# Performance work log

Hardware: AMD Instinct MI355X
Metric: run time of the kernel (lower is better)

The kernel has to match this reference:

```python
import jax, jax.numpy as jnp
import numpy as np

EPS = 1e-6
ROPE_THETA = 1000000.0

def _rmsnorm(x, scale):
    var = jnp.mean(jnp.square(x), axis=-1, keepdims=True)
    return x * jax.lax.rsqrt(var + EPS) * scale

def _rope(x, positions):
    # x: [B, h, T, H]; GPT-NeoX style rotate-half
    H = x.shape[-1]
    half = H // 2
    inv_freq = 1.0 / (ROPE_THETA ** (jnp.arange(half, dtype=jnp.float32) * 2.0 / H))
    ang = positions.astype(jnp.float32)[:, None] * inv_freq[None, :]  # [T, half]
    cos, sin = jnp.cos(ang), jnp.sin(ang)
    x1, x2 = x[..., :half], x[..., half:]
    return jnp.concatenate([x1 * cos - x2 * sin, x2 * cos + x1 * sin], axis=-1)

def setup_inputs() -> dict:
    key = jax.random.key(0)
    ks = jax.random.split(key, 16)
    B, T, D = 2, 2048, 2048
    N, K, H = 16, 2, 128
    I = 5504
    s = 0.02
    return {
        "x": jax.random.normal(ks[0], (B, T, D), jnp.float32),
        "positions": jnp.arange(T, dtype=jnp.int32),
        "ln1_scale": jnp.ones((D,), jnp.float32),
        "q_w": jax.random.normal(ks[1], (N, D, H), jnp.float32) * s,
        "q_b": jax.random.normal(ks[2], (N, H), jnp.float32) * s,
        "k_w": jax.random.normal(ks[3], (K, D, H), jnp.float32) * s,
        "k_b": jax.random.normal(ks[4], (K, H), jnp.float32) * s,
        "v_w": jax.random.normal(ks[5], (K, D, H), jnp.float32) * s,
        "v_b": jax.random.normal(ks[6], (K, H), jnp.float32) * s,
        "o_w": jax.random.normal(ks[7], (N, H, D), jnp.float32) * s,
        "ln2_scale": jnp.ones((D,), jnp.float32),
        "gate_w": jax.random.normal(ks[8], (D, I), jnp.float32) * s,
        "up_w": jax.random.normal(ks[9], (D, I), jnp.float32) * s,
        "down_w": jax.random.normal(ks[10], (I, D), jnp.float32) * s,
    }

def reference(x, positions, ln1_scale, q_w, q_b, k_w, k_b, v_w, v_b, o_w,
              ln2_scale, gate_w, up_w, down_w):
    B, T, D = x.shape
    N, _, H = q_w.shape
    K = k_w.shape[0]
    group = N // K

    h = _rmsnorm(x, ln1_scale)

    # Projections (per source einsums) + bias
    q = jnp.einsum('btd,ndh->bnth', h, q_w) + q_b[None, :, None, :]
    k = jnp.einsum('btd,kdh->bkth', h, k_w) + k_b[None, :, None, :]
    v = jnp.einsum('btd,kdh->bkth', h, v_w) + v_b[None, :, None, :]

    q = _rope(q, positions) * (H ** -0.5)
    k = _rope(k, positions)

    # GQA: expand kv heads to query heads
    k = jnp.repeat(k, group, axis=1)  # [B,N,T,H]
    v = jnp.repeat(v, group, axis=1)

    # Causal self-attention (prefill path: kv cache filled from k, v)
    scores = jnp.einsum('bnth,bnsh->bnts', q, k)
    causal = positions[:, None] >= positions[None, :]  # [T, T]
    scores = jnp.where(causal[None, None, :, :], scores, -jnp.inf)
    probs = jax.nn.softmax(scores, axis=-1)
    attn = jnp.einsum('bnts,bnsh->bnth', probs, v)

    o = jnp.einsum('bnth,nhd->btd', attn, o_w)

    # Residual + post-attn norm + SwiGLU MLP + residual
    res = o + x
    h2 = _rmsnorm(res, ln2_scale)
    fuse = jax.nn.silu(h2 @ gate_w) * (h2 @ up_w)
    return res + fuse @ down_w
```

## Files before the change

### kernel.cpp

```cpp
#include <hip/hip_runtime.h>
#include <cstdint>
#include <cstddef>

typedef unsigned short u16;
typedef __attribute__((ext_vector_type(8))) short short8;
typedef __attribute__((ext_vector_type(4))) float f32x4;

#define DEV __device__ __forceinline__

DEV float bf2f(u16 v) { union { unsigned u; float f; } x; x.u = ((unsigned)v) << 16; return x.f; }
DEV u16 f2bf(float f) {
  union { float f; unsigned u; } x; x.f = f;
  unsigned r = x.u + 0x7fffu + ((x.u >> 16) & 1u);
  return (u16)(r >> 16);
}

DEV void gload_lds16(const void* g, void* l) {
  __builtin_amdgcn_global_load_lds((const __attribute__((address_space(1))) void*)g,
                                   (__attribute__((address_space(3))) void*)l, 16, 0, 0);
}

#define BARRIER __builtin_amdgcn_s_barrier()
#define VM0 asm volatile("s_waitcnt vmcnt(0)" ::: "memory")
#define VM4 asm volatile("s_waitcnt vmcnt(4)" ::: "memory")

__global__ __launch_bounds__(256) void transpose_w_kernel(
    const float* __restrict__ in, u16* __restrict__ out, int R, int C, int mode)
{
  __shared__ float tile[64][65];
  const int tx = threadIdx.x, ty = threadIdx.y;
  const int c0 = blockIdx.x * 64, r0 = blockIdx.y * 64;
  const float* inb = in + (size_t)blockIdx.z * R * C;
  u16* outb = out + (size_t)blockIdx.z * R * C;
#pragma unroll
  for (int i = 0; i < 8; ++i) {
    const int r = ty + i * 8;
    const float2 v = *(const float2*)&inb[(size_t)(r0 + r) * C + c0 + tx * 2];
    tile[r][tx * 2] = v.x;
    tile[r][tx * 2 + 1] = v.y;
  }
  __syncthreads();
#pragma unroll
  for (int i = 0; i < 8; ++i) {
    const int jj = ty + i * 8;
    const int j = c0 + jj;
    const int prow = mode ? ((j >> 7) * 256 + (((j >> 5) & 3) << 6) + ((mode == 2) << 5) + (j & 31))
                          : j;
    const unsigned a = f2bf(tile[tx * 2][jj]);
    const unsigned b = f2bf(tile[tx * 2 + 1][jj]);
    *(unsigned*)&outb[(size_t)prow * R + r0 + tx * 2] = a | (b << 16);
  }
}

__global__ __launch_bounds__(256) void concat_bias_kernel(
    const float* __restrict__ qb, const float* __restrict__ kb,
    const float* __restrict__ vb, float* __restrict__ bias)
{
  const int i = blockIdx.x * 256 + threadIdx.x;
  if (i < 2048) bias[i] = qb[i];
  else if (i < 2304) bias[i] = kb[i - 2048];
  else if (i < 2560) bias[i] = vb[i - 2304];
}

__global__ __launch_bounds__(256) void rmsnorm_kernel(
    const float* __restrict__ x, const float* __restrict__ scale, u16* __restrict__ out)
{
  const int row = blockIdx.x, tid = threadIdx.x;
  const float* xr = x + (size_t)row * 2048;
  const float4 v0 = *(const float4*)&xr[tid * 8];
  const float4 v1 = *(const float4*)&xr[tid * 8 + 4];
  float ss = v0.x * v0.x + v0.y * v0.y + v0.z * v0.z + v0.w * v0.w +
             v1.x * v1.x + v1.y * v1.y + v1.z * v1.z + v1.w * v1.w;
#pragma unroll
  for (int d = 32; d > 0; d >>= 1) ss += __shfl_down(ss, d);
  __shared__ float red[4];
  if ((tid & 63) == 0) red[tid >> 6] = ss;
  __syncthreads();
  const float tot = red[0] + red[1] + red[2] + red[3];
  const float inv = rsqrtf(tot * (1.f / 2048.f) + 1e-6f);
  const float* sc = scale + tid * 8;
  short8 ov;
  ov[0] = (short)f2bf(v0.x * inv * sc[0]); ov[1] = (short)f2bf(v0.y * inv * sc[1]);
  ov[2] = (short)f2bf(v0.z * inv * sc[2]); ov[3] = (short)f2bf(v0.w * inv * sc[3]);
  ov[4] = (short)f2bf(v1.x * inv * sc[4]); ov[5] = (short)f2bf(v1.y * inv * sc[5]);
  ov[6] = (short)f2bf(v1.z * inv * sc[6]); ov[7] = (short)f2bf(v1.w * inv * sc[7]);
  *(short8*)&out[(size_t)row * 2048 + tid * 8] = ov;
}

template <int BM, int BN, int TB, int MODE, int GR>
__global__ __launch_bounds__(TB, 512 / TB) void gemm_conv_kernel(
    const u16* __restrict__ A, const u16* __restrict__ Bt,
    void* C, const float* __restrict__ aux, int N, int K, int lda, int ldb)
{
  constexpr int MFRAG = BM / 32;
  constexpr int AISS = BM * 8 / TB;
  constexpr int BISS = BN * 8 / TB;
  constexpr int WN = BN / 64;
  __shared__ __align__(16) u16 As[2][BM * 64];
  __shared__ __align__(16) u16 Bs[3][BN * 64];

  const int tid = threadIdx.x;
  const int wv = tid >> 6, lane = tid & 63, lo = lane & 15, hi = lane >> 4;
  const int wm = wv / WN, wn = wv % WN;

  const int nwg = (int)gridDim.x;
  const int id0 = (int)blockIdx.x;
  const int id = (id0 & 7) * (nwg >> 3) + (id0 >> 3);
  const int ncol = N / BN;
  const int rg = id % GR, cc = (id / GR) % ncol, gg = id / (GR * ncol);
  const int by = gg * GR + rg, bx = cc;
  const int row0 = by * BM, col0 = bx * BN;

  const f32x4 fz = {0.f, 0.f, 0.f, 0.f};
  f32x4 acc[MFRAG][4];
#pragma unroll
  for (int m = 0; m < MFRAG; ++m)
#pragma unroll
    for (int n = 0; n < 4; ++n) acc[m][n] = fz;

  const int nt = K >> 6;

  auto STAGE_A = [&](int kt, int ab) {
#pragma unroll
    for (int i = 0; i < AISS; ++i) {
      const int f = i * TB + tid;
      const int rp = f >> 3, sp = tid & 7;
      gload_lds16(A + (size_t)(row0 + rp) * lda + kt * 64 + ((sp ^ (rp & 7)) * 8),
                  (char*)&As[ab][0] + (i * TB + wv * 64) * 16);
    }
  };
  auto STAGE_B = [&](int kt, int bb) {
#pragma unroll
    for (int i = 0; i < BISS; ++i) {
      const int f = i * TB + tid;
      const int rp = f >> 3, sp = tid & 7;
      gload_lds16(Bt + (size_t)(col0 + rp) * ldb + kt * 64 + ((sp ^ (rp & 7)) * 8),
                  (char*)&Bs[bb][0] + (i * TB + wv * 64) * 16);
    }
  };

#define LDA8M(ARR, BUF, S, G)                                                    \
  _Pragma("unroll")                                                              \
  for (int mt = 0; mt < 4; ++mt) {                                               \
    const int r = wm * (BM / 2) + ((G) * 4 + mt) * 16 + lo;                      \
    ARR[mt] = *(const short8*)&As[BUF][r * 64 + (((S) * 4 + hi) ^ (r & 7)) * 8]; \
  }
#define LDB8M(ARR, BUF, S)                                                       \
  _Pragma("unroll")                                                              \
  for (int nn = 0; nn < 4; ++nn) {                                               \
    const int r = wn * 64 + nn * 16 + lo;                                        \
    ARR[nn] = *(const short8*)&Bs[BUF][r * 64 + (((S) * 4 + hi) ^ (r & 7)) * 8]; \
  }
#define MFMA16M(AR, BR, G)                                                       \
  __builtin_amdgcn_s_setprio(1);                                                 \
  _Pragma("unroll")                                                              \
  for (int mt = 0; mt < 4; ++mt)                                                 \
    _Pragma("unroll")                                                            \
    for (int nn = 0; nn < 4; ++nn)                                               \
      acc[(G) * 4 + mt][nn] = __builtin_amdgcn_mfma_f32_16x16x32_bf16(           \
          AR[mt], BR[nn], acc[(G) * 4 + mt][nn], 0, 0, 0);                       \
  __builtin_amdgcn_s_setprio(0);

  STAGE_A(0, 0); STAGE_B(0, 0); STAGE_B(1, 1);
  VM4; BARRIER;

  int ab = 0, bcur = 0;
  for (int t = 0; t < nt; ++t) {
    const bool preA = (t + 1 < nt);
    const bool preB = (t + 2 < nt);
    const int bs2 = (bcur >= 1) ? bcur - 1 : 2;
    if constexpr (BM == 256) {
      short8 a0[4], a1[4], b0[4], a2[4], a3[4], b1[4];
      LDA8M(a0, ab, 0, 0); LDA8M(a1, ab, 0, 1); LDB8M(b0, bcur, 0);
      LDA8M(a2, ab, 1, 0); LDA8M(a3, ab, 1, 1); LDB8M(b1, bcur, 1);
      if (preA) STAGE_A(t + 1, ab ^ 1);
      if (preB) STAGE_B(t + 2, bs2);
      MFMA16M(a0, b0, 0); MFMA16M(a1, b0, 1);
      MFMA16M(a2, b1, 0); MFMA16M(a3, b1, 1);
      if (preA) { if (preB) VM4; else VM0; }
      BARRIER;
    } else {
      short8 a0[4], b0[4], a1[4], b1[4];
      LDA8M(a0, ab, 0, 0); LDB8M(b0, bcur, 0);
      LDA8M(a1, ab, 1, 0); LDB8M(b1, bcur, 1);
      if (preA) STAGE_A(t + 1, ab ^ 1);
      if (preB) STAGE_B(t + 2, bs2);
      MFMA16M(a0, b0, 0);
      MFMA16M(a1, b1, 0);
      if (preA) { if (preB) VM4; else VM0; }
      BARRIER;
    }
    ab ^= 1;
    bcur = (bcur == 2) ? 0 : bcur + 1;
  }
#undef LDA8M
#undef LDB8M
#undef MFMA16M

  float* Cf = (float*)C;
  u16* Ch = (u16*)C;
  if constexpr (MODE == 4) {
    const int ldo = N >> 1;
#pragma unroll
    for (int fm = 0; fm < MFRAG; ++fm) {
#pragma unroll
      for (int nn = 0; nn < 2; ++nn) {
        const int fcol = (col0 >> 1) + wn * 32 + nn * 16 + lo;
#pragma unroll
        for (int j = 0; j < 4; ++j) {
          const int row = row0 + wm * (BM / 2) + fm * 16 + hi * 4 + j;
          const float g = acc[fm][nn][j];
          const float u = acc[fm][nn + 2][j];
          const float sg = g / (1.f + __builtin_amdgcn_exp2f(-1.4426950408889634f * g));
          Ch[(size_t)row * ldo + fcol] = f2bf(sg * u);
        }
      }
    }
  } else {
#pragma unroll
    for (int fm = 0; fm < MFRAG; ++fm) {
#pragma unroll
      for (int nn = 0; nn < 4; ++nn) {
        const int col = col0 + wn * 64 + nn * 16 + lo;
#pragma unroll
        for (int j = 0; j < 4; ++j) {
          const int row = row0 + wm * (BM / 2) + fm * 16 + hi * 4 + j;
          const size_t idx = (size_t)row * N + col;
          const float v = acc[fm][nn][j];
          if (MODE == 0) Cf[idx] = v + aux[col];
          else if (MODE == 1) Cf[idx] = v + aux[idx];
          else if (MODE == 2) Ch[idx] = f2bf(v);
          else Ch[idx] = f2bf(v + aux[col]);
        }
      }
    }
  }
}

__global__ __launch_bounds__(256) void rope_qkv_kernel(
    const u16* __restrict__ qkv, const int* __restrict__ pos,
    u16* __restrict__ Qb, u16* __restrict__ Kb, u16* __restrict__ Vt)
{
  const int idx = blockIdx.x * 256 + threadIdx.x;
  const int bt = idx / 1408;
  const int r = idx - bt * 1408;
  const int t = bt & 2047, b = bt >> 11;
  if (r < 1152) {
    const bool isq = r < 1024;
    const int rr = isq ? r : r - 1024;
    const int n = rr >> 6, hp = rr & 63;
    const u16* q = qkv + (size_t)bt * 2560 + (isq ? 0 : 2048) + n * 128 + hp;
    const float x1 = bf2f(q[0]);
    const float x2 = bf2f(q[64]);
    const float inv = exp2f((float)hp * (-19.931568569324174f / 64.f));
    const float ang = (float)pos[t] * inv;
    float s, c;
    sincosf(ang, &s, &c);
    const float sc = isq ? 0.08838834764831845f * 1.4426950408889634f : 1.f;
    const size_t base = isq ? (((size_t)(b * 16 + n) * 2048 + t) * 128 + hp)
                            : (((size_t)(b * 2 + n) * 2048 + t) * 128 + hp);
    u16* outp = isq ? Qb : Kb;
    outp[base] = f2bf((x1 * c - x2 * s) * sc);
    outp[base + 64] = f2bf((x2 * c + x1 * s) * sc);
  } else {
    const int rr = r - 1152;
    const int kh = rr >> 7, hh = rr & 127;
    Vt[((size_t)((b * 2 + kh) * 128 + hh)) * 2048 + t] =
        qkv[(size_t)bt * 2560 + 2304 + kh * 128 + hh];
  }
}

__global__ __launch_bounds__(512) void attn_kernel(
    const u16* __restrict__ Qb, const u16* __restrict__ Kb,
    const u16* __restrict__ Vt, u16* __restrict__ Out)
{
  __shared__ u16 Ks[2][128 * 128];
  __shared__ u16 Vs[2][128 * 128];
  __shared__ u16 Ps[8][16 * 128];
  const int tid = threadIdx.x;
  const int wave = tid >> 6, lane = tid & 63, lo = lane & 15, hi = lane >> 4;
  const int bn = blockIdx.x;
  const int b = bn >> 4, n = bn & 15, kh = n >> 3;

  const f32x4 fz = {0.f, 0.f, 0.f, 0.f};
  const u16* kg = Kb + (size_t)(b * 2 + kh) * 2048 * 128;
  const u16* vg = Vt + (size_t)(b * 2 + kh) * 128 * 2048;

  auto STAGE = [&](int buf, int s0) {
#pragma unroll
    for (int i = 0; i < 4; ++i) {
      const int gk = i * 512 + tid;
      const int rk = gk >> 4, gck = gk & 15;
      gload_lds16(kg + (size_t)(s0 + rk) * 128 + ((gck ^ (rk & 7)) * 8),
                  (char*)&Ks[buf][0] + (i * 512 + wave * 64) * 16);
      gload_lds16(vg + (size_t)rk * 2048 + s0 + ((gck ^ (rk & 7)) * 8),
                  (char*)&Vs[buf][0] + (i * 512 + wave * 64) * 16);
    }
  };

  auto processTile = [&](int q0) {
    const int nblk = q0 / 128 + 1;
    const u16* qptr = Qb + ((size_t)((b * 16 + n) * 2048) + q0 + wave * 16 + lo) * 128;
    short8 qf[4];
#pragma unroll
    for (int kc = 0; kc < 4; ++kc) qf[kc] = *(const short8*)&qptr[kc * 32 + hi * 8];

    float m_r[4], l_r[4];
    f32x4 oacc[8];
#pragma unroll
    for (int j = 0; j < 4; ++j) { m_r[j] = -1e30f; l_r[j] = 0.f; }
#pragma unroll
    for (int ht = 0; ht < 8; ++ht) oacc[ht] = fz;

    __syncthreads();
    STAGE(0, 0);
    __syncthreads();

    int cur = 0;
    for (int sb = 0; sb < nblk; ++sb) {
      const int s0 = sb * 128;
      if (sb + 1 < nblk) STAGE(cur ^ 1, s0 + 128);

      float sall[8][4];
      __builtin_amdgcn_s_setprio(1);
#pragma unroll
      for (int st = 0; st < 8; ++st) {
        f32x4 s = fz;
#pragma unroll
        for (int kc = 0; kc < 4; ++kc) {
          const int row = st * 16 + lo;
          const int cb = (kc * 64 + hi * 16) ^ ((lo & 7) << 4);
          short8 kf = *(const short8*)&Ks[cur][row * 128 + (cb >> 1)];
          s = __builtin_amdgcn_mfma_f32_16x16x32_bf16(qf[kc], kf, s, 0, 0, 0);
        }
#pragma unroll
        for (int j = 0; j < 4; ++j) sall[st][j] = s[j];
      }
      __builtin_amdgcn_s_setprio(0);

      if (s0 + 128 > q0) {
#pragma unroll
        for (int st = 0; st < 8; ++st) {
          const int sg = s0 + st * 16 + lo;
#pragma unroll
          for (int j = 0; j < 4; ++j) {
            const int qg = q0 + wave * 16 + hi * 4 + j;
            if (sg > qg) sall[st][j] = -1e30f;
          }
        }
      }

      float tmax[4];
#pragma unroll
      for (int j = 0; j < 4; ++j) {
        float t = fmaxf(fmaxf(fmaxf(sall[0][j], sall[1][j]), fmaxf(sall[2][j], sall[3][j])),
                        fmaxf(fmaxf(sall[4][j], sall[5][j]), fmaxf(sall[6][j], sall[7][j])));
        t = fmaxf(t, __shfl_xor(t, 1));
        t = fmaxf(t, __shfl_xor(t, 2));
        t = fmaxf(t, __shfl_xor(t, 4));
        t = fmaxf(t, __shfl_xor(t, 8));
        tmax[j] = t;
      }
      const bool defer = __all((tmax[0] - m_r[0] <= 8.f) & (tmax[1] - m_r[1] <= 8.f) &
                               (tmax[2] - m_r[2] <= 8.f) & (tmax[3] - m_r[3] <= 8.f));
      if (!defer) {
        float alpha[4];
#pragma unroll
        for (int j = 0; j < 4; ++j) {
          const float mnew = fmaxf(m_r[j], tmax[j]);
          alpha[j] = __builtin_amdgcn_exp2f(m_r[j] - mnew);
          m_r[j] = mnew;
          l_r[j] *= alpha[j];
        }
#pragma unroll
        for (int ht = 0; ht < 8; ++ht) {
#pragma unroll
          for (int j = 0; j < 4; ++j) oacc[ht][j] *= alpha[j];
        }
      }

      float rsum[4] = {0.f, 0.f, 0.f, 0.f};
#pragma unroll
      for (int st = 0; st < 8; ++st) {
#pragma unroll
        for (int j = 0; j < 4; ++j) {
          const float p = __builtin_amdgcn_exp2f(sall[st][j] - m_r[j]);
          rsum[j] += p;
          const int row = hi * 4 + j;
          const int cbp = (st * 32 + lo * 2) ^ ((row & 7) << 4);
          Ps[wave][row * 128 + (cbp >> 1)] = f2bf(p);
        }
      }
#pragma unroll
      for (int j = 0; j < 4; ++j) {
        float rs = rsum[j];
        rs += __shfl_xor(rs, 1);
        rs += __shfl_xor(rs, 2);
        rs += __shfl_xor(rs, 4);
        rs += __shfl_xor(rs, 8);
        l_r[j] += rs;
      }

      asm volatile("s_waitcnt lgkmcnt(0)" ::: "memory");
      __builtin_amdgcn_sched_barrier(0);

      short8 pf[4];
#pragma unroll
      for (int s = 0; s < 4; ++s) {
        const int pcb = (s * 64 + hi * 16) ^ ((lo & 7) << 4);
        pf[s] = *(const short8*)&Ps[wave][lo * 128 + (pcb >> 1)];
      }
      __builtin_amdgcn_s_setprio(1);
#pragma unroll
      for (int ht = 0; ht < 8; ++ht) {
        const int row = ht * 16 + lo;
#pragma unroll
        for (int s = 0; s < 4; ++s) {
          const int cb = (s * 64 + hi * 16) ^ ((row & 7) << 4);
          const short8 vf = *(const short8*)&Vs[cur][row * 128 + (cb >> 1)];
          oacc[ht] = __builtin_amdgcn_mfma_f32_16x16x32_bf16(pf[s], vf, oacc[ht], 0, 0, 0);
        }
      }
      __builtin_amdgcn_s_setprio(0);

      if (sb + 1 < nblk) __syncthreads();
      cur ^= 1;
    }

#pragma unroll
    for (int j = 0; j < 4; ++j) {
      const float inv = 1.0f / l_r[j];
      const int trow = q0 + wave * 16 + hi * 4 + j;
      const size_t base = ((size_t)(b * 2048 + trow)) * 2048 + n * 128;
#pragma unroll
      for (int ht = 0; ht < 8; ++ht)
        Out[base + ht * 16 + lo] = f2bf(oacc[ht][j] * inv);
    }
  };

  processTile((int)(15 - blockIdx.y) * 128);
  processTile((int)blockIdx.y * 128);
}

extern "C" void kernel_launch(void* const* d_in, const int* in_sizes, int n_in,
                              void* d_out, int out_size, void* d_ws, size_t ws_size,
                              hipStream_t stream)
{
  const float* x      = (const float*)d_in[0];
  const int*   pos    = (const int*)d_in[1];
  const float* ln1    = (const float*)d_in[2];
  const float* q_w    = (const float*)d_in[3];
  const float* q_b    = (const float*)d_in[4];
  const float* k_w    = (const float*)d_in[5];
  const float* k_b    = (const float*)d_in[6];
  const float* v_w    = (const float*)d_in[7];
  const float* v_b    = (const float*)d_in[8];
  const float* o_w    = (const float*)d_in[9];
  const float* ln2    = (const float*)d_in[10];
  const float* gate_w = (const float*)d_in[11];
  const float* up_w   = (const float*)d_in[12];
  const float* down_w = (const float*)d_in[13];
  float* out = (float*)d_out;

  char* w = (char*)d_ws;
  u16* wqkv_t = (u16*)w;       w += 2560LL * 2048 * 2;
  u16* o_wt   = (u16*)w;       w += 2048LL * 2048 * 2;
  u16* gu_t   = (u16*)w;       w += 11008LL * 2048 * 2;
  u16* d_t    = (u16*)w;       w += 2048LL * 5504 * 2;
  u16* hbuf   = (u16*)w;       w += 4096LL * 2048 * 2;
  float* bias_qkv = (float*)w; w += 2560 * 4;
  char* un = w;
  u16*  qkv   = (u16*)un;
  u16*  Qb    = (u16*)(un + 41943040LL);
  u16*  Kb    = (u16*)(un + 41943040LL + 16777216LL);
  u16*  Vt    = (u16*)(un + 41943040LL + 16777216LL + 2097152LL);
  u16*  attnb = (u16*)(un + 41943040LL + 16777216LL + 2097152LL + 2097152LL);
  u16*  fusebuf = (u16*)un;

  const dim3 tb(32, 8);
  transpose_w_kernel<<<dim3(2, 32, 16), tb, 0, stream>>>(q_w, wqkv_t, 2048, 128, 0);
  transpose_w_kernel<<<dim3(2, 32, 2),  tb, 0, stream>>>(k_w, wqkv_t + 2048LL * 2048, 2048, 128, 0);
  transpose_w_kernel<<<dim3(2, 32, 2),  tb, 0, stream>>>(v_w, wqkv_t + 2304LL * 2048, 2048, 128, 0);
  transpose_w_kernel<<<dim3(32, 32, 1), tb, 0, stream>>>(o_w, o_wt, 2048, 2048, 0);
  transpose_w_kernel<<<dim3(86, 32, 1), tb, 0, stream>>>(gate_w, gu_t, 2048, 5504, 1);
  transpose_w_kernel<<<dim3(86, 32, 1), tb, 0, stream>>>(up_w, gu_t, 2048, 5504, 2);
  transpose_w_kernel<<<dim3(32, 86, 1), tb, 0, stream>>>(down_w, d_t, 5504, 2048, 0);
  concat_bias_kernel<<<10, 256, 0, stream>>>(q_b, k_b, v_b, bias_qkv);

  rmsnorm_kernel<<<4096, 256, 0, stream>>>(x, ln1, hbuf);
  gemm_conv_kernel<128, 128, 256, 3, 8><<<640, 256, 0, stream>>>(hbuf, wqkv_t, qkv, bias_qkv, 2560, 2048, 2048, 2048);
  rope_qkv_kernel<<<22528, 256, 0, stream>>>(qkv, pos, Qb, Kb, Vt);
  attn_kernel<<<dim3(32, 8), 512, 0, stream>>>(Qb, Kb, Vt, attnb);
  gemm_conv_kernel<128, 128, 256, 1, 8><<<512, 256, 0, stream>>>(attnb, o_wt, out, x, 2048, 2048, 2048, 2048);
  rmsnorm_kernel<<<4096, 256, 0, stream>>>(out, ln2, hbuf);
  gemm_conv_kernel<256, 256, 512, 4, 4><<<688, 512, 0, stream>>>(hbuf, gu_t, fusebuf, nullptr, 11008, 2048, 2048, 2048);
  gemm_conv_kernel<128, 128, 256, 1, 2><<<512, 256, 0, stream>>>(fusebuf, d_t, out, out, 2048, 5504, 5504, 5504);
}
```

Measured before the change: 532.5 us.

## Switch GEMM inner loop to 32x32x16 bf16 MFMA with per-k-step fragment loads

Replaces the 16x16x32 MFMA tiling in the shared GEMM kernel with 32x32x16 MFMAs on 16-float accumulators, loading A/B fragments per k-substep of 16. The larger MFMA shape reuses each fragment load across more output elements, cutting LDS reads per flop. The epilogues are remapped to the 32x32 output layout. The down-projection launch also changes its row-group swizzle from 2 to 8, which alters L2 reuse.

```diff
diff --git a/kernel.cpp b/kernel.cpp
--- a/kernel.cpp
+++ b/kernel.cpp
@@ -5,6 +5,7 @@
 typedef unsigned short u16;
 typedef __attribute__((ext_vector_type(8))) short short8;
 typedef __attribute__((ext_vector_type(4))) float f32x4;
+typedef __attribute__((ext_vector_type(16))) float f32x16;
 
 #define DEV __device__ __forceinline__
 
@@ -92,15 +93,18 @@
     const u16* __restrict__ A, const u16* __restrict__ Bt,
     void* C, const float* __restrict__ aux, int N, int K, int lda, int ldb)
 {
-  constexpr int MFRAG = BM / 32;
+  constexpr int WN = BN / 64;
+  constexpr int NWM = (TB / 64) / WN;
+  constexpr int PWM = BM / NWM;
+  constexpr int AF = PWM / 32;
   constexpr int AISS = BM * 8 / TB;
   constexpr int BISS = BN * 8 / TB;
-  constexpr int WN = BN / 64;
   __shared__ __align__(16) u16 As[2][BM * 64];
   __shared__ __align__(16) u16 Bs[3][BN * 64];
 
   const int tid = threadIdx.x;
-  const int wv = tid >> 6, lane = tid & 63, lo = lane & 15, hi = lane >> 4;
+  const int wv = tid >> 6, lane = tid & 63;
+  const int l31 = lane & 31, l5 = lane >> 5;
   const int wm = wv / WN, wn = wv % WN;
 
   const int nwg = (int)gridDim.x;
@@ -111,12 +115,13 @@
   const int by = gg * GR + rg, bx = cc;
   const int row0 = by * BM, col0 = bx * BN;
 
-  const f32x4 fz = {0.f, 0.f, 0.f, 0.f};
-  f32x4 acc[MFRAG][4];
-#pragma unroll
-  for (int m = 0; m < MFRAG; ++m)
-#pragma unroll
-    for (int n = 0; n < 4; ++n) acc[m][n] = fz;
+  f32x16 acc[AF][2];
+#pragma unroll
+  for (int m = 0; m < AF; ++m)
+#pragma unroll
+    for (int n = 0; n < 2; ++n)
+#pragma unroll
+      for (int e = 0; e < 16; ++e) acc[m][n][e] = 0.f;
 
   const int nt = K >> 6;
 
@@ -139,28 +144,6 @@
     }
   };
 
-#define LDA8M(ARR, BUF, S, G)                                                    \
-  _Pragma("unroll")                                                              \
-  for (int mt = 0; mt < 4; ++mt) {                                               \
-    const int r = wm * (BM / 2) + ((G) * 4 + mt) * 16 + lo;                      \
-    ARR[mt] = *(const short8*)&As[BUF][r * 64 + (((S) * 4 + hi) ^ (r & 7)) * 8]; \
-  }
-#define LDB8M(ARR, BUF, S)                                                       \
-  _Pragma("unroll")                                                              \
-  for (int nn = 0; nn < 4; ++nn) {                                               \
-    const int r = wn * 64 + nn * 16 + lo;                                        \
-    ARR[nn] = *(const short8*)&Bs[BUF][r * 64 + (((S) * 4 + hi) ^ (r & 7)) * 8]; \
-  }
-#define MFMA16M(AR, BR, G)                                                       \
-  __builtin_amdgcn_s_setprio(1);                                                 \
-  _Pragma("unroll")                                                              \
-  for (int mt = 0; mt < 4; ++mt)                                                 \
-    _Pragma("unroll")                                                            \
-    for (int nn = 0; nn < 4; ++nn)                                               \
-      acc[(G) * 4 + mt][nn] = __builtin_amdgcn_mfma_f32_16x16x32_bf16(           \
-          AR[mt], BR[nn], acc[(G) * 4 + mt][nn], 0, 0, 0);                       \
-  __builtin_amdgcn_s_setprio(0);
-
   STAGE_A(0, 0); STAGE_B(0, 0); STAGE_B(1, 1);
   VM4; BARRIER;
 
@@ -169,64 +152,66 @@
     const bool preA = (t + 1 < nt);
     const bool preB = (t + 2 < nt);
     const int bs2 = (bcur >= 1) ? bcur - 1 : 2;
-    if constexpr (BM == 256) {
-      short8 a0[4], a1[4], b0[4], a2[4], a3[4], b1[4];
-      LDA8M(a0, ab, 0, 0); LDA8M(a1, ab, 0, 1); LDB8M(b0, bcur, 0);
-      LDA8M(a2, ab, 1, 0); LDA8M(a3, ab, 1, 1); LDB8M(b1, bcur, 1);
-      if (preA) STAGE_A(t + 1, ab ^ 1);
-      if (preB) STAGE_B(t + 2, bs2);
-      MFMA16M(a0, b0, 0); MFMA16M(a1, b0, 1);
-      MFMA16M(a2, b1, 0); MFMA16M(a3, b1, 1);
-      if (preA) { if (preB) VM4; else VM0; }
-      BARRIER;
-    } else {
-      short8 a0[4], b0[4], a1[4], b1[4];
-      LDA8M(a0, ab, 0, 0); LDB8M(b0, bcur, 0);
-      LDA8M(a1, ab, 1, 0); LDB8M(b1, bcur, 1);
-      if (preA) STAGE_A(t + 1, ab ^ 1);
-      if (preB) STAGE_B(t + 2, bs2);
-      MFMA16M(a0, b0, 0);
-      MFMA16M(a1, b1, 0);
-      if (preA) { if (preB) VM4; else VM0; }
-      BARRIER;
-    }
+#pragma unroll
+    for (int ks = 0; ks < 4; ++ks) {
+      short8 a[AF], b[2];
+#pragma unroll
+      for (int af = 0; af < AF; ++af) {
+        const int r = wm * PWM + af * 32 + l31;
+        a[af] = *(const short8*)&As[ab][r * 64 + (((ks * 2 + l5)) ^ (r & 7)) * 8];
+      }
+#pragma unroll
+      for (int bf = 0; bf < 2; ++bf) {
+        const int r = wn * 64 + bf * 32 + l31;
+        b[bf] = *(const short8*)&Bs[bcur][r * 64 + (((ks * 2 + l5)) ^ (r & 7)) * 8];
+      }
+      if (ks == 0) {
+        if (preA) STAGE_A(t + 1, ab ^ 1);
+        if (preB) STAGE_B(t + 2, bs2);
+      }
+      __builtin_amdgcn_s_setprio(1);
+#pragma unroll
+      for (int af = 0; af < AF; ++af) {
+#pragma unroll
+        for (int bf = 0; bf < 2; ++bf)
+          acc[af][bf] = __builtin_amdgcn_mfma_f32_32x32x16_bf16(
+              a[af], b[bf], acc[af][bf], 0, 0, 0);
+      }
+      __builtin_amdgcn_s_setprio(0);
+    }
+    if (preA) { if (preB) VM4; else VM0; }
+    BARRIER;
     ab ^= 1;
     bcur = (bcur == 2) ? 0 : bcur + 1;
   }
-#undef LDA8M
-#undef LDB8M
-#undef MFMA16M
 
   float* Cf = (float*)C;
   u16* Ch = (u16*)C;
   if constexpr (MODE == 4) {
     const int ldo = N >> 1;
-#pragma unroll
-    for (int fm = 0; fm < MFRAG; ++fm) {
-#pragma unroll
-      for (int nn = 0; nn < 2; ++nn) {
-        const int fcol = (col0 >> 1) + wn * 32 + nn * 16 + lo;
-#pragma unroll
-        for (int j = 0; j < 4; ++j) {
-          const int row = row0 + wm * (BM / 2) + fm * 16 + hi * 4 + j;
-          const float g = acc[fm][nn][j];
-          const float u = acc[fm][nn + 2][j];
-          const float sg = g / (1.f + __builtin_amdgcn_exp2f(-1.4426950408889634f * g));
-          Ch[(size_t)row * ldo + fcol] = f2bf(sg * u);
-        }
+    const int fcol = (col0 >> 1) + wn * 32 + l31;
+#pragma unroll
+    for (int af = 0; af < AF; ++af) {
+#pragma unroll
+      for (int reg = 0; reg < 16; ++reg) {
+        const int row = row0 + wm * PWM + af * 32 + (reg & 3) + 8 * (reg >> 2) + 4 * l5;
+        const float g = acc[af][0][reg];
+        const float u = acc[af][1][reg];
+        const float sg = g / (1.f + __builtin_amdgcn_exp2f(-1.4426950408889634f * g));
+        Ch[(size_t)row * ldo + fcol] = f2bf(sg * u);
       }
     }
   } else {
 #pragma unroll
-    for (int fm = 0; fm < MFRAG; ++fm) {
-#pragma unroll
-      for (int nn = 0; nn < 4; ++nn) {
-        const int col = col0 + wn * 64 + nn * 16 + lo;
-#pragma unroll
-        for (int j = 0; j < 4; ++j) {
-          const int row = row0 + wm * (BM / 2) + fm * 16 + hi * 4 + j;
+    for (int af = 0; af < AF; ++af) {
+#pragma unroll
+      for (int bf = 0; bf < 2; ++bf) {
+        const int col = col0 + wn * 64 + bf * 32 + l31;
+#pragma unroll
+        for (int reg = 0; reg < 16; ++reg) {
+          const int row = row0 + wm * PWM + af * 32 + (reg & 3) + 8 * (reg >> 2) + 4 * l5;
           const size_t idx = (size_t)row * N + col;
-          const float v = acc[fm][nn][j];
+          const float v = acc[af][bf][reg];
           if (MODE == 0) Cf[idx] = v + aux[col];
           else if (MODE == 1) Cf[idx] = v + aux[idx];
           else if (MODE == 2) Ch[idx] = f2bf(v);
@@ -494,5 +479,5 @@
   gemm_conv_kernel<128, 128, 256, 1, 8><<<512, 256, 0, stream>>>(attnb, o_wt, out, x, 2048, 2048, 2048, 2048);
   rmsnorm_kernel<<<4096, 256, 0, stream>>>(out, ln2, hbuf);
   gemm_conv_kernel<256, 256, 512, 4, 4><<<688, 512, 0, stream>>>(hbuf, gu_t, fusebuf, nullptr, 11008, 2048, 2048, 2048);
-  gemm_conv_kernel<128, 128, 256, 1, 2><<<512, 256, 0, stream>>>(fusebuf, d_t, out, out, 2048, 5504, 5504, 5504);
-}
+  gemm_conv_kernel<128, 128, 256, 1, 8><<<512, 256, 0, stream>>>(fusebuf, d_t, out, out, 2048, 5504, 5504, 5504);
+}
```

Measured after the change: 605.9 us. 1.14x slower.
